# Performance work log

Hardware: AMD Instinct MI355X
Metric: run time of the kernel (lower is better)

Reference implementation:

```python
import jax, jax.numpy as jnp
import numpy as np

LOG2PI = float(np.log(2.0 * np.pi))
T, S, D, K = 1024, 512, 32, 64


def setup_inputs() -> dict:
    key = jax.random.key(0)
    k0, k1, k2, k3, k4 = jax.random.split(key, 5)
    data = jax.random.normal(k0, (T, S, D), dtype=jnp.float32)  # packed time-major
    ip = jax.random.uniform(k1, (K,), dtype=jnp.float32)
    initial_probs = ip / ip.sum()
    A = jax.random.uniform(k2, (K, K), dtype=jnp.float32)
    transition_probs = A / A.sum(-1, keepdims=True)  # row-stochastic
    means = jax.random.normal(k3, (K, D), dtype=jnp.float32)
    covars = jax.random.uniform(k4, (K, D), dtype=jnp.float32) * 0.5 + 0.5  # positive diag
    return {"data": data, "initial_probs": initial_probs,
            "transition_probs": transition_probs, "means": means, "covars": covars}


def _emission_probs(data, means, covars):
    # Gaussian diag-covariance densities, [T, S, K], without materializing [T,S,K,D].
    inv = 1.0 / covars  # [K, D]
    quad = (jnp.einsum('tsd,kd->tsk', data * data, inv)
            - 2.0 * jnp.einsum('tsd,kd->tsk', data, means * inv)
            + (means * means * inv).sum(-1))  # [T, S, K]
    logp = -0.5 * (quad + jnp.log(covars).sum(-1) + data.shape[-1] * LOG2PI)
    return jnp.exp(logp)


def reference(data, initial_probs, transition_probs, means, covars):
    probs = _emission_probs(data, means, covars)  # [T, S, K]
    # t = 0: alpha = normalize(initial * emission)
    a0 = initial_probs * probs[0]
    d0 = a0.sum(-1, keepdims=True)
    alpha0 = a0 / d0
    log_denom0 = jnp.log(d0)  # [S, 1]

    def step(carry, p_t):
        alpha, log_denom = carry
        a = p_t * (alpha @ transition_probs)  # [S, K]
        d = a.sum(-1, keepdims=True)
        return (a / d, log_denom + jnp.log(d)), None

    (alpha, log_denom), _ = jax.lax.scan(step, (alpha0, log_denom0), probs[1:])
    log_likeli = jax.nn.logsumexp(jnp.log(alpha) + log_denom, axis=-1).sum()
    return alpha, -log_likeli
```

## Files before the change

### kernel.cpp

```cpp
#include <hip/hip_runtime.h>
#include <hip/hip_fp16.h>
#include <math.h>

#define TT 1024
#define SS 512
#define DD 32
#define KK 64

#define LOG2PI_F 1.8378770664093453f
#define L2E_F    1.4426950408889634f
#define LN2_F    0.6931471805599453f

#define QSEQ 16
#define NSEG 32
#define SEGLEN (TT / NSEG)
#define BURN 64

#define PBUF_BYTES ((size_t)TT * SS * KK * 2)
#define EM_WPB 4
#define EM_BLOCKS 2048
#define NWAVES (EM_BLOCKS * EM_WPB)

typedef float v2f __attribute__((ext_vector_type(2)));
typedef float f32x4 __attribute__((ext_vector_type(4)));
typedef _Float16 h8 __attribute__((ext_vector_type(8)));

__device__ __forceinline__ v2f fma2(v2f a, v2f b, v2f c) {
#if __has_builtin(__builtin_elementwise_fma)
    return __builtin_elementwise_fma(a, b, c);
#else
    v2f r; r.x = fmaf(a.x, b.x, c.x); r.y = fmaf(a.y, b.y, c.y); return r;
#endif
}

__device__ __forceinline__ float fast_exp2(float x) {
#if __has_builtin(__builtin_amdgcn_exp2f)
    return __builtin_amdgcn_exp2f(x);
#else
    return __expf(x * LN2_F);
#endif
}

template <int CTRL, int RMASK>
__device__ __forceinline__ float dpp_max(float x) {
    int xi = __float_as_int(x);
    int t = __builtin_amdgcn_update_dpp(xi, xi, CTRL, RMASK, 0xf, false);
    return fmaxf(x, __int_as_float(t));
}
__device__ __forceinline__ float wave_reduce_max(float x) {
    x = dpp_max<0x111, 0xf>(x);
    x = dpp_max<0x112, 0xf>(x);
    x = dpp_max<0x114, 0xf>(x);
    x = dpp_max<0x118, 0xf>(x);
    x = dpp_max<0x142, 0xa>(x);
    x = dpp_max<0x143, 0xc>(x);
    return __int_as_float(__builtin_amdgcn_readlane(__float_as_int(x), 63));
}
template <int N>
__device__ __forceinline__ float dpp_ror_add(float x) {
    int xi = __float_as_int(x);
    int t = __builtin_amdgcn_update_dpp(xi, xi, 0x120 + N, 0xf, 0xf, false);
    return x + __int_as_float(t);
}
__device__ __forceinline__ float rowsum16(float x) {
    x = dpp_ror_add<8>(x);
    x = dpp_ror_add<4>(x);
    x = dpp_ror_add<2>(x);
    x = dpp_ror_add<1>(x);
    return x;
}

__global__ __launch_bounds__(EM_WPB * 64)
__attribute__((amdgpu_waves_per_eu(1, 3)))
void emission_kernel(
    const float* __restrict__ data,
    const float* __restrict__ means,
    const float* __restrict__ covars,
    __half* __restrict__ pbuf,
    float* __restrict__ mpart)
{
    const int k  = threadIdx.x & 63;
    const int w  = threadIdx.x >> 6;
    const int wv = blockIdx.x * EM_WPB + w;

    v2f W2[DD / 2], MW2[DD / 2];
    float c0 = DD * LOG2PI_F;
    float mm = 0.0f;
#pragma unroll
    for (int d = 0; d < DD; ++d) {
        float c = covars[k * DD + d];
        float m = means[k * DD + d];
        float wi = 1.0f / c;
        ((float*)W2)[d]  = -0.5f * L2E_F * wi;
        ((float*)MW2)[d] = L2E_F * wi * m;
        mm += m * m * wi;
        c0 += __logf(c);
    }
    const float C = -0.5f * L2E_F * (c0 + mm);

    __shared__ __align__(16) float4 xst[EM_WPB][2][64];
    __shared__ __align__(16) float4 sst[EM_WPB][2][64];

    const int base = wv * 64;
    const float4* dsrc = (const float4*)(data + (size_t)base * DD);

    float4 xr = dsrc[k];
    float4 sr; sr.x = xr.x * xr.x; sr.y = xr.y * xr.y;
    sr.z = xr.z * xr.z; sr.w = xr.w * xr.w;
    xst[w][0][k] = xr;
    sst[w][0][k] = sr;
    __builtin_amdgcn_wave_barrier();

    float macc = 0.0f;
    int cur = 0;

    for (int b = 0; b < 8; ++b) {
        const int bn = (b + 1 < 8) ? (b + 1) : 7;
        xr = dsrc[bn * 64 + k];

        const float* xb = (const float*)&xst[w][cur][0];
        const float* sb = (const float*)&sst[w][cur][0];
#pragma unroll
        for (int i = 0; i < 8; ++i) {
            const int item = base + b * 8 + i;
            const float4* xq = (const float4*)(xb + i * DD);
            const float4* sq = (const float4*)(sb + i * DD);
            v2f qa = {C, 0.0f}, qb = {0.0f, 0.0f};
            v2f qc = {0.0f, 0.0f}, qd = {0.0f, 0.0f};
#pragma unroll
            for (int d4 = 0; d4 < DD / 4; ++d4) {
                float4 xv = xq[d4];
                float4 sv = sq[d4];
                v2f x01; x01.x = xv.x; x01.y = xv.y;
                v2f x23; x23.x = xv.z; x23.y = xv.w;
                v2f s01; s01.x = sv.x; s01.y = sv.y;
                v2f s23; s23.x = sv.z; s23.y = sv.w;
                qa = fma2(s01, W2[2 * d4], qa);
                qb = fma2(s23, W2[2 * d4 + 1], qb);
                qc = fma2(x01, MW2[2 * d4], qc);
                qd = fma2(x23, MW2[2 * d4 + 1], qd);
            }
            v2f s = (qa + qb) + (qc + qd);
            float logp2 = s.x + s.y;
            float mx2 = wave_reduce_max(logp2);
            pbuf[(size_t)item * KK + k] = __float2half(fast_exp2(logp2 - mx2));
            macc += mx2;
        }

        float4 s2; s2.x = xr.x * xr.x; s2.y = xr.y * xr.y;
        s2.z = xr.z * xr.z; s2.w = xr.w * xr.w;
        xst[w][cur ^ 1][k] = xr;
        sst[w][cur ^ 1][k] = s2;
        __builtin_amdgcn_wave_barrier();
        cur ^= 1;
    }
    if (k == 0) mpart[wv] = macc;
}

#define RSTR 72

__global__ __launch_bounds__(64)
__attribute__((amdgpu_waves_per_eu(1, 1)))
void hmm_mfma(
    const __half* __restrict__ pbuf,
    const float* __restrict__ initial,
    const float* __restrict__ trans,
    float* __restrict__ out_alpha,
    float* __restrict__ seq_logd)
{
    const int lane = threadIdx.x;
    const int col  = lane & 15;
    const int grp  = lane >> 4;
    const int s0   = blockIdx.x * QSEQ;
    const int seg  = blockIdx.y;

    const int emit_from = seg * SEGLEN;
    int t0 = emit_from - BURN; if (t0 < 0) t0 = 0;
    const int nsteps = (emit_from - t0) + SEGLEN;

    h8 bf[2][4];
#pragma unroll
    for (int kc = 0; kc < 2; ++kc)
#pragma unroll
        for (int nt = 0; nt < 4; ++nt) {
            h8 v;
#pragma unroll
            for (int e = 0; e < 8; ++e) {
                int j = kc * 32 + grp * 8 + e;
                v[e] = (_Float16)trans[j * KK + nt * 16 + col];
            }
            bf[kc][nt] = v;
        }

    float init_c[4];
#pragma unroll
    for (int nt = 0; nt < 4; ++nt)
        init_c[nt] = (t0 == 0) ? initial[nt * 16 + col] : 1.0f;

    __shared__ __align__(16) _Float16 ash[QSEQ * RSTR];
    __shared__ __align__(16) _Float16 plds[2][4 * QSEQ * RSTR];

    float4 pr[8];
#define XLOAD(TB)                                                             \
    {                                                                         \
        const float4* src = (const float4*)(pbuf +                            \
            (((size_t)((TB) + grp)) * SS + s0 + col) * KK);                   \
        _Pragma("unroll")                                                     \
        for (int e = 0; e < 8; ++e) pr[e] = src[e];                           \
    }
#define XWRITE(BUF)                                                           \
    {                                                                         \
        float4* dst = (float4*)(&plds[BUF][(grp * 16 + col) * RSTR]);         \
        _Pragma("unroll")                                                     \
        for (int e = 0; e < 8; ++e) dst[e] = pr[e];                           \
    }

    XLOAD(t0);
    XWRITE(0);
    __builtin_amdgcn_wave_barrier();

    h8 a0, a1;
    float ld[4] = {0.0f, 0.0f, 0.0f, 0.0f};
    int cur = 0;

    for (int g = 0; g < nsteps / 4; ++g) {
        const int tbase = t0 + 4 * g;
        int tb_next = tbase + 4;
        if (tb_next > TT - 4) tb_next = TT - 4;
        XLOAD(tb_next);

        const _Float16* pc_base = &plds[cur][0];
#pragma unroll
        for (int st = 0; st < 4; ++st) {
            const int t = tbase + st;
            f32x4 c[4];
            if (g == 0 && st == 0) {
#pragma unroll
                for (int nt = 0; nt < 4; ++nt) {
                    f32x4 z = {init_c[nt], init_c[nt], init_c[nt], init_c[nt]};
                    c[nt] = z;
                }
            } else {
                f32x4 z = {0.0f, 0.0f, 0.0f, 0.0f};
#pragma unroll
                for (int nt = 0; nt < 4; ++nt) {
                    c[nt] = __builtin_amdgcn_mfma_f32_16x16x32_f16(
                        a0, bf[0][nt], z, 0, 0, 0);
                    c[nt] = __builtin_amdgcn_mfma_f32_16x16x32_f16(
                        a1, bf[1][nt], c[nt], 0, 0, 0);
                }
            }

            float av[4][4];
            float pden[4] = {0.0f, 0.0f, 0.0f, 0.0f};
#pragma unroll
            for (int nt = 0; nt < 4; ++nt)
#pragma unroll
                for (int j = 0; j < 4; ++j) {
                    float pcv = (float)pc_base[
                        (st * 16 + grp * 4 + j) * RSTR + nt * 16 + col];
                    float v = c[nt][j] * pcv;
                    av[nt][j] = v;
                    pden[j] += v;
                }

            float r[4];
#pragma unroll
            for (int j = 0; j < 4; ++j) {
                float den = rowsum16(pden[j]);
                if (t >= emit_from) ld[j] += __logf(den);
                r[j] = __builtin_amdgcn_rcpf(den);
            }

#pragma unroll
            for (int nt = 0; nt < 4; ++nt)
#pragma unroll
                for (int j = 0; j < 4; ++j)
                    ash[(grp * 4 + j) * RSTR + nt * 16 + col] =
                        (_Float16)(av[nt][j] * r[j]);
            __builtin_amdgcn_wave_barrier();
            a0 = *(const h8*)(ash + col * RSTR + grp * 8);
            a1 = *(const h8*)(ash + col * RSTR + 32 + grp * 8);
            __builtin_amdgcn_wave_barrier();
        }

        XWRITE(cur ^ 1);
        __builtin_amdgcn_wave_barrier();
        cur ^= 1;
    }
#undef XLOAD
#undef XWRITE

    if (seg == NSEG - 1) {
#pragma unroll
        for (int nt = 0; nt < 4; ++nt)
#pragma unroll
            for (int j = 0; j < 4; ++j)
                out_alpha[(size_t)(s0 + grp * 4 + j) * KK + nt * 16 + col] =
                    (float)ash[(grp * 4 + j) * RSTR + nt * 16 + col];
    }
    if (col == 0) {
#pragma unroll
        for (int j = 0; j < 4; ++j)
            seq_logd[seg * SS + s0 + grp * 4 + j] = ld[j];
    }
}

__global__ __launch_bounds__(256) void finalize(
    const float* __restrict__ seq_logd, const float* __restrict__ mpart,
    float* __restrict__ out_nll)
{
    float v = 0.0f;
    for (int j = threadIdx.x; j < NWAVES; j += 256) v += mpart[j] * LN2_F;
    for (int j = threadIdx.x; j < NSEG * SS; j += 256) v += seq_logd[j];
#pragma unroll
    for (int off = 32; off > 0; off >>= 1)
        v += __shfl_xor(v, off, 64);
    __shared__ float sh[4];
    if ((threadIdx.x & 63) == 0) sh[threadIdx.x >> 6] = v;
    __syncthreads();
    if (threadIdx.x == 0) {
        double total = ((double)sh[0] + sh[1]) + ((double)sh[2] + sh[3]);
        out_nll[0] = (float)(-total);
    }
}

extern "C" void kernel_launch(void* const* d_in, const int* in_sizes, int n_in,
                              void* d_out, int out_size, void* d_ws, size_t ws_size,
                              hipStream_t stream) {
    const float* data    = (const float*)d_in[0];
    const float* initial = (const float*)d_in[1];
    const float* trans   = (const float*)d_in[2];
    const float* means   = (const float*)d_in[3];
    const float* covars  = (const float*)d_in[4];

    float* out_alpha = (float*)d_out;
    float* out_nll   = (float*)d_out + (size_t)SS * KK;

    __half* pbuf     = (__half*)d_ws;
    float*  mpart    = (float*)((char*)d_ws + PBUF_BYTES);
    float*  seq_logd = (float*)((char*)d_ws + PBUF_BYTES + NWAVES * sizeof(float));

    emission_kernel<<<EM_BLOCKS, EM_WPB * 64, 0, stream>>>(
        data, means, covars, pbuf, mpart);
    hmm_mfma<<<dim3(SS / QSEQ, NSEG), 64, 0, stream>>>(
        pbuf, initial, trans, out_alpha, seq_logd);
    finalize<<<1, 256, 0, stream>>>(seq_logd, mpart, out_nll);
}
```

Measured before the change: 275.1 us.

## Restructure emission kernel to one item per lane with precomputed Gaussian tables

Switches the emission kernel from one lane per state (with a cross-lane max reduction per item) to one lane per (t,s) item. Each lane loops over all 64 states, reading means and inverse variances from a small precomputed table produced by a new prep kernel. Log-probabilities go to shared memory, the per-item max is taken serially, and fp16 probabilities are written as 16-byte vector stores. This removes the per-item wave reductions and the scalar half stores, at the cost of an extra tiny launch, broadcast global table loads inside the inner loop, and computing (x-m)^2*w directly.

```diff
diff --git a/kernel.cpp b/kernel.cpp
--- a/kernel.cpp
+++ b/kernel.cpp
@@ -17,9 +17,9 @@
 #define BURN 64
 
 #define PBUF_BYTES ((size_t)TT * SS * KK * 2)
-#define EM_WPB 4
-#define EM_BLOCKS 2048
-#define NWAVES (EM_BLOCKS * EM_WPB)
+#define NWAVES 8192
+#define EM_TBL 68
+#define LP_STR 65
 
 typedef float v2f __attribute__((ext_vector_type(2)));
 typedef float f32x4 __attribute__((ext_vector_type(4)));
@@ -42,18 +42,17 @@
 }
 
 template <int CTRL, int RMASK>
-__device__ __forceinline__ float dpp_max(float x) {
-    int xi = __float_as_int(x);
-    int t = __builtin_amdgcn_update_dpp(xi, xi, CTRL, RMASK, 0xf, false);
-    return fmaxf(x, __int_as_float(t));
-}
-__device__ __forceinline__ float wave_reduce_max(float x) {
-    x = dpp_max<0x111, 0xf>(x);
-    x = dpp_max<0x112, 0xf>(x);
-    x = dpp_max<0x114, 0xf>(x);
-    x = dpp_max<0x118, 0xf>(x);
-    x = dpp_max<0x142, 0xa>(x);
-    x = dpp_max<0x143, 0xc>(x);
+__device__ __forceinline__ float dpp_add_bc(float x) {
+    int t = __builtin_amdgcn_update_dpp(0, __float_as_int(x), CTRL, RMASK, 0xf, true);
+    return x + __int_as_float(t);
+}
+__device__ __forceinline__ float wave_reduce_sum(float x) {
+    x = dpp_add_bc<0x111, 0xf>(x);
+    x = dpp_add_bc<0x112, 0xf>(x);
+    x = dpp_add_bc<0x114, 0xf>(x);
+    x = dpp_add_bc<0x118, 0xf>(x);
+    x = dpp_add_bc<0x142, 0xa>(x);
+    x = dpp_add_bc<0x143, 0xc>(x);
     return __int_as_float(__builtin_amdgcn_readlane(__float_as_int(x), 63));
 }
 template <int N>
@@ -70,91 +69,108 @@
     return x;
 }
 
-__global__ __launch_bounds__(EM_WPB * 64)
-__attribute__((amdgpu_waves_per_eu(1, 3)))
+__global__ __launch_bounds__(64) void prep_kernel(
+    const float* __restrict__ means, const float* __restrict__ covars,
+    float* __restrict__ tables)
+{
+    const int k = threadIdx.x;
+    float acc = DD * LOG2PI_F;
+    for (int d = 0; d < DD; ++d) {
+        float c = covars[k * DD + d];
+        tables[k * EM_TBL + d]      = means[k * DD + d];
+        tables[k * EM_TBL + 32 + d] = -0.5f * L2E_F / c;
+        acc += __logf(c);
+    }
+    tables[k * EM_TBL + 64] = -0.5f * L2E_F * acc;
+}
+
+__global__ __launch_bounds__(64)
+__attribute__((amdgpu_waves_per_eu(1, 2)))
 void emission_kernel(
     const float* __restrict__ data,
-    const float* __restrict__ means,
-    const float* __restrict__ covars,
+    const float* __restrict__ tables,
     __half* __restrict__ pbuf,
     float* __restrict__ mpart)
 {
-    const int k  = threadIdx.x & 63;
-    const int w  = threadIdx.x >> 6;
-    const int wv = blockIdx.x * EM_WPB + w;
-
-    v2f W2[DD / 2], MW2[DD / 2];
-    float c0 = DD * LOG2PI_F;
-    float mm = 0.0f;
-#pragma unroll
-    for (int d = 0; d < DD; ++d) {
-        float c = covars[k * DD + d];
-        float m = means[k * DD + d];
-        float wi = 1.0f / c;
-        ((float*)W2)[d]  = -0.5f * L2E_F * wi;
-        ((float*)MW2)[d] = L2E_F * wi * m;
-        mm += m * m * wi;
-        c0 += __logf(c);
-    }
-    const float C = -0.5f * L2E_F * (c0 + mm);
-
-    __shared__ __align__(16) float4 xst[EM_WPB][2][64];
-    __shared__ __align__(16) float4 sst[EM_WPB][2][64];
-
-    const int base = wv * 64;
-    const float4* dsrc = (const float4*)(data + (size_t)base * DD);
-
-    float4 xr = dsrc[k];
-    float4 sr; sr.x = xr.x * xr.x; sr.y = xr.y * xr.y;
-    sr.z = xr.z * xr.z; sr.w = xr.w * xr.w;
-    xst[w][0][k] = xr;
-    sst[w][0][k] = sr;
+    const int l  = threadIdx.x;
+    const int wv = blockIdx.x;
+    const int item = wv * 64 + l;
+
+    __shared__ float lp[64 * LP_STR];
+
+    v2f xv[DD / 2];
+    {
+        const float4* xp = (const float4*)(data + (size_t)item * DD);
+#pragma unroll
+        for (int j = 0; j < DD / 4; ++j) {
+            float4 x = xp[j];
+            v2f a; a.x = x.x; a.y = x.y;
+            v2f b; b.x = x.z; b.y = x.w;
+            xv[2 * j] = a; xv[2 * j + 1] = b;
+        }
+    }
+
+    for (int k = 0; k < KK; ++k) {
+        const float* tb = tables + k * EM_TBL;
+        const float4* mq = (const float4*)tb;
+        const float4* wq = (const float4*)(tb + 32);
+        float C2 = tb[64];
+        v2f q0 = {0.0f, 0.0f}, q1 = {0.0f, 0.0f};
+        v2f q2 = {0.0f, 0.0f}, q3 = {0.0f, 0.0f};
+        q0.x = C2;
+#pragma unroll
+        for (int j = 0; j < DD / 8; ++j) {
+            float4 mv0 = mq[2 * j], mv1 = mq[2 * j + 1];
+            float4 wv0 = wq[2 * j], wv1 = wq[2 * j + 1];
+            v2f m01; m01.x = mv0.x; m01.y = mv0.y;
+            v2f m23; m23.x = mv0.z; m23.y = mv0.w;
+            v2f m45; m45.x = mv1.x; m45.y = mv1.y;
+            v2f m67; m67.x = mv1.z; m67.y = mv1.w;
+            v2f w01; w01.x = wv0.x; w01.y = wv0.y;
+            v2f w23; w23.x = wv0.z; w23.y = wv0.w;
+            v2f w45; w45.x = wv1.x; w45.y = wv1.y;
+            v2f w67; w67.x = wv1.z; w67.y = wv1.w;
+            v2f t0 = xv[4 * j]     - m01;
+            v2f t1 = xv[4 * j + 1] - m23;
+            v2f t2 = xv[4 * j + 2] - m45;
+            v2f t3 = xv[4 * j + 3] - m67;
+            q0 = fma2(w01 * t0, t0, q0);
+            q1 = fma2(w23 * t1, t1, q1);
+            q2 = fma2(w45 * t2, t2, q2);
+            q3 = fma2(w67 * t3, t3, q3);
+        }
+        v2f s = (q0 + q1) + (q2 + q3);
+        lp[l * LP_STR + k] = s.x + s.y;
+    }
     __builtin_amdgcn_wave_barrier();
 
-    float macc = 0.0f;
-    int cur = 0;
-
-    for (int b = 0; b < 8; ++b) {
-        const int bn = (b + 1 < 8) ? (b + 1) : 7;
-        xr = dsrc[bn * 64 + k];
-
-        const float* xb = (const float*)&xst[w][cur][0];
-        const float* sb = (const float*)&sst[w][cur][0];
-#pragma unroll
-        for (int i = 0; i < 8; ++i) {
-            const int item = base + b * 8 + i;
-            const float4* xq = (const float4*)(xb + i * DD);
-            const float4* sq = (const float4*)(sb + i * DD);
-            v2f qa = {C, 0.0f}, qb = {0.0f, 0.0f};
-            v2f qc = {0.0f, 0.0f}, qd = {0.0f, 0.0f};
-#pragma unroll
-            for (int d4 = 0; d4 < DD / 4; ++d4) {
-                float4 xv = xq[d4];
-                float4 sv = sq[d4];
-                v2f x01; x01.x = xv.x; x01.y = xv.y;
-                v2f x23; x23.x = xv.z; x23.y = xv.w;
-                v2f s01; s01.x = sv.x; s01.y = sv.y;
-                v2f s23; s23.x = sv.z; s23.y = sv.w;
-                qa = fma2(s01, W2[2 * d4], qa);
-                qb = fma2(s23, W2[2 * d4 + 1], qb);
-                qc = fma2(x01, MW2[2 * d4], qc);
-                qd = fma2(x23, MW2[2 * d4 + 1], qd);
-            }
-            v2f s = (qa + qb) + (qc + qd);
-            float logp2 = s.x + s.y;
-            float mx2 = wave_reduce_max(logp2);
-            pbuf[(size_t)item * KK + k] = __float2half(fast_exp2(logp2 - mx2));
-            macc += mx2;
-        }
-
-        float4 s2; s2.x = xr.x * xr.x; s2.y = xr.y * xr.y;
-        s2.z = xr.z * xr.z; s2.w = xr.w * xr.w;
-        xst[w][cur ^ 1][k] = xr;
-        sst[w][cur ^ 1][k] = s2;
-        __builtin_amdgcn_wave_barrier();
-        cur ^= 1;
-    }
-    if (k == 0) mpart[wv] = macc;
+    const float* row = lp + l * LP_STR;
+    float m0 = row[0], m1 = row[1], m2 = row[2], m3 = row[3];
+#pragma unroll
+    for (int j = 4; j < KK; j += 4) {
+        m0 = fmaxf(m0, row[j]);
+        m1 = fmaxf(m1, row[j + 1]);
+        m2 = fmaxf(m2, row[j + 2]);
+        m3 = fmaxf(m3, row[j + 3]);
+    }
+    const float mx2 = fmaxf(fmaxf(m0, m1), fmaxf(m2, m3));
+
+    __half* pb = pbuf + (size_t)item * KK;
+#pragma unroll
+    for (int c = 0; c < 8; ++c) {
+        unsigned int out[4];
+#pragma unroll
+        for (int e = 0; e < 4; ++e) {
+            float e0 = fast_exp2(row[c * 8 + 2 * e]     - mx2);
+            float e1 = fast_exp2(row[c * 8 + 2 * e + 1] - mx2);
+            __half2 h = __halves2half2(__float2half(e0), __float2half(e1));
+            out[e] = *(unsigned int*)&h;
+        }
+        *(float4*)(pb + c * 8) = *(float4*)out;
+    }
+
+    float ms = wave_reduce_sum(mx2);
+    if (l == 0) mpart[wv] = ms;
 }
 
 #define RSTR 72
@@ -340,9 +356,11 @@
     __half* pbuf     = (__half*)d_ws;
     float*  mpart    = (float*)((char*)d_ws + PBUF_BYTES);
     float*  seq_logd = (float*)((char*)d_ws + PBUF_BYTES + NWAVES * sizeof(float));
-
-    emission_kernel<<<EM_BLOCKS, EM_WPB * 64, 0, stream>>>(
-        data, means, covars, pbuf, mpart);
+    float*  tables   = (float*)((char*)d_ws + PBUF_BYTES + NWAVES * sizeof(float)
+                                + NSEG * SS * sizeof(float));
+
+    prep_kernel<<<1, 64, 0, stream>>>(means, covars, tables);
+    emission_kernel<<<NWAVES, 64, 0, stream>>>(data, tables, pbuf, mpart);
     hmm_mfma<<<dim3(SS / QSEQ, NSEG), 64, 0, stream>>>(
         pbuf, initial, trans, out_alpha, seq_logd);
     finalize<<<1, 256, 0, stream>>>(seq_logd, mpart, out_nll);
```

Result: no change. 280.3 us (+1.9%).
